# Kernel tuning notes

Measured on AMD Instinct MI355X. Metric: run time of the kernel, lower is better.

Reference implementation:

```python
import jax, jax.numpy as jnp
import numpy as np

N_ROIS = 8192
C, S = 256, 7
D = C * S * S  # 12544 flattened RoI feature dim
NUM_CLASSES = 31
DIMS = {"cls": NUM_CLASSES + 1, "reg": 4 * NUM_CLASSES, "face": 3, "colour": 7, "motion": 2}


def setup_inputs() -> dict:
    key = jax.random.key(0)
    ks = jax.random.split(key, 6)
    x = jax.random.normal(ks[0], (N_ROIS, C, S, S), dtype=jnp.float32)
    inp = {"x": x}
    for i, (name, out_dim) in enumerate(DIMS.items()):
        inp[f"W_{name}"] = 0.01 * jax.random.normal(ks[i + 1], (D, out_dim), dtype=jnp.float32)
        inp[f"b_{name}"] = jnp.zeros((out_dim,), dtype=jnp.float32)
    return inp


def reference(x, W_cls, b_cls, W_reg, b_reg, W_face, b_face,
              W_colour, b_colour, W_motion, b_motion):
    # AttributeBBoxHead.forward with with_avg_pool=False: flatten then 5 linear heads.
    xf = x.reshape(x.shape[0], -1)  # (N, 12544)
    cls_score = xf @ W_cls + b_cls        # (N, 32)
    bbox_pred = xf @ W_reg + b_reg        # (N, 124)
    face_score = xf @ W_face + b_face     # (N, 3)
    colour_score = xf @ W_colour + b_colour  # (N, 7)
    motion_score = xf @ W_motion + b_motion  # (N, 2)
    return (cls_score, bbox_pred, face_score, colour_score, motion_score)
```

## Files before the change

### kernel.cpp

```cpp
#include <hip/hip_runtime.h>
#include <hip/hip_bf16.h>
#include <stdint.h>

#define D_DIM 12544
#define NROIS 8192
#define NCOLS 168
#define NCPAD 176
#define NT 11
#define SPLIT 8
#define KSPLIT (D_DIM / SPLIT)
#define BK 32
#define KITERS (KSPLIT / BK)
#define BM 64

#define XROW_B 72
#define WCOL_B 80
#define WL_COLS 192
#define XL_BYTES (BM * XROW_B)
#define WL_BYTES (WL_COLS * WCOL_B)
#define BUF_BYTES (XL_BYTES + WL_BYTES)

typedef __attribute__((ext_vector_type(8))) short short8;
typedef __attribute__((ext_vector_type(4))) float floatx4;

__device__ __forceinline__ uint32_t pk_bf16(float a, float b) {
    uint32_t ua = __float_as_uint(a);
    uint32_t ub = __float_as_uint(b);
    ua = (ua + 0x7FFFu + ((ua >> 16) & 1u)) >> 16;
    ub = (ub + 0x7FFFu + ((ub >> 16) & 1u)) >> 16;
    return ua | (ub << 16);
}

__global__ __launch_bounds__(256) void pack_w(
        const float* __restrict__ Wc, const float* __restrict__ Wr,
        const float* __restrict__ Wf, const float* __restrict__ Wco,
        const float* __restrict__ Wm, uint16_t* __restrict__ Wp) {
    __shared__ float tile[64][33];
    int k0 = blockIdx.x * 64;
    int c0 = blockIdx.y * 32;
    int t  = threadIdx.x;

    int rc = t & 31;
    int rk = t >> 5;
#pragma unroll
    for (int rr = 0; rr < 8; ++rr) {
        int k = rr * 8 + rk;
        int kk = k0 + k;
        int c = c0 + rc;
        float v = 0.f;
        if (c < 32)       v = Wc[(size_t)kk * 32  + c];
        else if (c < 156) v = Wr[(size_t)kk * 124 + (c - 32)];
        else if (c < 159) v = Wf[(size_t)kk * 3   + (c - 156)];
        else if (c < 166) v = Wco[(size_t)kk * 7  + (c - 159)];
        else if (c < 168) v = Wm[(size_t)kk * 2   + (c - 166)];
        tile[k][rc] = v;
    }
    __syncthreads();

    int wc = t >> 3;
    int wk = t & 7;
    int c  = c0 + wc;
    if (c < NCPAD) {
        uint32_t o[4];
#pragma unroll
        for (int j = 0; j < 4; ++j)
            o[j] = pk_bf16(tile[wk * 8 + 2 * j][wc], tile[wk * 8 + 2 * j + 1][wc]);
        uint4 v = make_uint4(o[0], o[1], o[2], o[3]);
        *(uint4*)(Wp + (size_t)c * D_DIM + k0 + wk * 8) = v;
    }
}

__global__ __launch_bounds__(256) void gemm_split(const float* __restrict__ X,
                                                  const uint16_t* __restrict__ Wp,
                                                  uint16_t* __restrict__ parts) {
    __shared__ __attribute__((aligned(16))) char lds[2 * BUF_BYTES];

    int b     = blockIdx.x;
    int split = b & 7;
    int rb    = b >> 3;
    int row0  = rb * BM;
    int kbase = split * KSPLIT;

    int t    = threadIdx.x;
    int wave = t >> 6;
    int lane = t & 63;

    int sx_row = t >> 2;
    int sx_kc  = t & 3;
    const float* xg = X + (size_t)(row0 + sx_row) * D_DIM + kbase + sx_kc * 8;

    int sw_col = t >> 2;
    int sw_ch  = t & 3;
    int c0g = sw_col       < NCPAD ? sw_col       : NCPAD - 1;
    int c1g = sw_col + 64  < NCPAD ? sw_col + 64  : NCPAD - 1;
    int c2g = sw_col + 128 < NCPAD ? sw_col + 128 : NCPAD - 1;
    const uint16_t* wg0 = Wp + (size_t)c0g * D_DIM + kbase + sw_ch * 8;
    const uint16_t* wg1 = Wp + (size_t)c1g * D_DIM + kbase + sw_ch * 8;
    const uint16_t* wg2 = Wp + (size_t)c2g * D_DIM + kbase + sw_ch * 8;

    int x_st = sx_row * XROW_B + sx_kc * 16;
    int w_st0 = XL_BYTES + (sw_col)       * WCOL_B + sw_ch * 16;
    int w_st1 = XL_BYTES + (sw_col + 64)  * WCOL_B + sw_ch * 16;
    int w_st2 = XL_BYTES + (sw_col + 128) * WCOL_B + sw_ch * 16;

    int n    = lane & 15;
    int quad = lane >> 4;
    int xf_off = (wave * 16 + n) * XROW_B + quad * 16;
    int wf_off = XL_BYTES + n * WCOL_B + quad * 16;

    floatx4 acc[NT];
#pragma unroll
    for (int tt = 0; tt < NT; ++tt) acc[tt] = (floatx4)0.f;

    float4 px0 = *(const float4*)xg;
    float4 px1 = *(const float4*)(xg + 4);
    xg += BK;
    short8 pw0 = *(const short8*)wg0; wg0 += BK;
    short8 pw1 = *(const short8*)wg1; wg1 += BK;
    short8 pw2 = *(const short8*)wg2; wg2 += BK;
    {
        union { uint32_t u[4]; short8 s; } p;
        p.u[0] = pk_bf16(px0.x, px0.y); p.u[1] = pk_bf16(px0.z, px0.w);
        p.u[2] = pk_bf16(px1.x, px1.y); p.u[3] = pk_bf16(px1.z, px1.w);
        *(short8*)(lds + x_st) = p.s;
        *(short8*)(lds + w_st0) = pw0;
        *(short8*)(lds + w_st1) = pw1;
        *(short8*)(lds + w_st2) = pw2;
    }
    int cur = 0;

    for (int it = 0; it < KITERS; ++it) {
        __syncthreads();

        float4 nx0, nx1; short8 nw0, nw1, nw2;
        bool more = (it + 1 < KITERS);
        if (more) {
            nx0 = *(const float4*)xg;
            nx1 = *(const float4*)(xg + 4);
            xg += BK;
            nw0 = *(const short8*)wg0; wg0 += BK;
            nw1 = *(const short8*)wg1; wg1 += BK;
            nw2 = *(const short8*)wg2; wg2 += BK;
        }

        const char* cb = lds + cur * BUF_BYTES;
        short8 xf = *(const short8*)(cb + xf_off);
#pragma unroll
        for (int tt = 0; tt < NT; ++tt) {
            short8 wf = *(const short8*)(cb + wf_off + tt * (16 * WCOL_B));
            acc[tt] = __builtin_amdgcn_mfma_f32_16x16x32_bf16(wf, xf, acc[tt], 0, 0, 0);
        }

        if (more) {
            char* nb = lds + (cur ^ 1) * BUF_BYTES;
            union { uint32_t u[4]; short8 s; } p;
            p.u[0] = pk_bf16(nx0.x, nx0.y); p.u[1] = pk_bf16(nx0.z, nx0.w);
            p.u[2] = pk_bf16(nx1.x, nx1.y); p.u[3] = pk_bf16(nx1.z, nx1.w);
            *(short8*)(nb + x_st) = p.s;
            *(short8*)(nb + w_st0) = nw0;
            *(short8*)(nb + w_st1) = nw1;
            *(short8*)(nb + w_st2) = nw2;
            cur ^= 1;
        }
    }

    uint16_t* pb = parts + ((size_t)split * NROIS + row0 + wave * 16 + n) * NCOLS;
#pragma unroll
    for (int tt = 0; tt < NT; ++tt) {
        int col0 = tt * 16 + quad * 4;
        if (col0 + 3 < NCOLS) {
            uint32_t lo = pk_bf16(acc[tt].x, acc[tt].y);
            uint32_t hi = pk_bf16(acc[tt].z, acc[tt].w);
            uint2 v = make_uint2(lo, hi);
            *(uint2*)(pb + col0) = v;
        }
    }
}

__global__ void reduce_out(const uint16_t* __restrict__ parts,
                           const float* __restrict__ bc, const float* __restrict__ br,
                           const float* __restrict__ bf, const float* __restrict__ bco,
                           const float* __restrict__ bm, float* __restrict__ out) {
    int r = blockIdx.x;
    int c = threadIdx.x;
    if (c >= NCOLS) return;
    const size_t S = (size_t)NROIS * NCOLS;
    size_t off = (size_t)r * NCOLS + c;
    float v = 0.f;
#pragma unroll
    for (int s = 0; s < SPLIT; ++s)
        v += __uint_as_float((uint32_t)parts[off + (size_t)s * S] << 16);
    float bias; size_t oidx;
    if (c < 32)       { bias = bc[c];        oidx = (size_t)r * 32  + c; }
    else if (c < 156) { bias = br[c - 32];   oidx = 262144u  + (size_t)r * 124 + (c - 32); }
    else if (c < 159) { bias = bf[c - 156];  oidx = 1277952u + (size_t)r * 3   + (c - 156); }
    else if (c < 166) { bias = bco[c - 159]; oidx = 1302528u + (size_t)r * 7   + (c - 159); }
    else              { bias = bm[c - 166];  oidx = 1359872u + (size_t)r * 2   + (c - 166); }
    out[oidx] = v + bias;
}

extern "C" void kernel_launch(void* const* d_in, const int* in_sizes, int n_in,
                              void* d_out, int out_size, void* d_ws, size_t ws_size,
                              hipStream_t stream) {
    const float* X   = (const float*)d_in[0];
    const float* Wc  = (const float*)d_in[1];
    const float* bc  = (const float*)d_in[2];
    const float* Wr  = (const float*)d_in[3];
    const float* br  = (const float*)d_in[4];
    const float* Wf  = (const float*)d_in[5];
    const float* bfa = (const float*)d_in[6];
    const float* Wco = (const float*)d_in[7];
    const float* bco = (const float*)d_in[8];
    const float* Wm  = (const float*)d_in[9];
    const float* bm  = (const float*)d_in[10];

    uint16_t* Wp    = (uint16_t*)d_ws;
    uint16_t* parts = (uint16_t*)((char*)d_ws + (size_t)NCPAD * D_DIM * 2);
    float* out = (float*)d_out;

    pack_w<<<dim3(D_DIM / 64, 6), 256, 0, stream>>>(Wc, Wr, Wf, Wco, Wm, Wp);
    gemm_split<<<1024, 256, 0, stream>>>(X, Wp, parts);
    reduce_out<<<NROIS, 192, 0, stream>>>(parts, bc, br, bfa, bco, bm, out);
}
```

Before: 608.8 us.

## Load X fragments directly to registers and fuse split-K reduction via tickets

X tiles are no longer staged through shared memory. Each lane loads its own MFMA fragment from global memory and converts it to bf16 in registers, which cuts LDS traffic and footprint. The separate reduce kernel is removed: each row block counts finished K-splits with an atomic ticket, and the last block sums the partials and adds bias. This saves a launch and a pass over partials, but adds fence and atomic overhead and leaves the final reduction to a single block per row group.

```diff
diff --git a/kernel.cpp b/kernel.cpp
--- a/kernel.cpp
+++ b/kernel.cpp
@@ -1,5 +1,4 @@
 #include <hip/hip_runtime.h>
-#include <hip/hip_bf16.h>
 #include <stdint.h>
 
 #define D_DIM 12544
@@ -12,13 +11,11 @@
 #define BK 32
 #define KITERS (KSPLIT / BK)
 #define BM 64
-
-#define XROW_B 72
+#define NRB (NROIS / BM)
+
 #define WCOL_B 80
 #define WL_COLS 192
-#define XL_BYTES (BM * XROW_B)
-#define WL_BYTES (WL_COLS * WCOL_B)
-#define BUF_BYTES (XL_BYTES + WL_BYTES)
+#define WBUF_BYTES (WL_COLS * WCOL_B)
 
 typedef __attribute__((ext_vector_type(8))) short short8;
 typedef __attribute__((ext_vector_type(4))) float floatx4;
@@ -34,11 +31,14 @@
 __global__ __launch_bounds__(256) void pack_w(
         const float* __restrict__ Wc, const float* __restrict__ Wr,
         const float* __restrict__ Wf, const float* __restrict__ Wco,
-        const float* __restrict__ Wm, uint16_t* __restrict__ Wp) {
+        const float* __restrict__ Wm, uint16_t* __restrict__ Wp,
+        uint32_t* __restrict__ tickets) {
     __shared__ float tile[64][33];
     int k0 = blockIdx.x * 64;
     int c0 = blockIdx.y * 32;
     int t  = threadIdx.x;
+
+    if (blockIdx.x == 0 && blockIdx.y == 0 && t < NRB) tickets[t] = 0;
 
     int rc = t & 31;
     int rk = t >> 5;
@@ -70,10 +70,14 @@
     }
 }
 
-__global__ __launch_bounds__(256) void gemm_split(const float* __restrict__ X,
-                                                  const uint16_t* __restrict__ Wp,
-                                                  uint16_t* __restrict__ parts) {
-    __shared__ __attribute__((aligned(16))) char lds[2 * BUF_BYTES];
+__global__ __launch_bounds__(256) void gemm_fused(
+        const float* __restrict__ X, const uint16_t* __restrict__ Wp,
+        uint16_t* __restrict__ parts, uint32_t* __restrict__ tickets,
+        const float* __restrict__ bc, const float* __restrict__ br,
+        const float* __restrict__ bfa, const float* __restrict__ bco,
+        const float* __restrict__ bm, float* __restrict__ out) {
+    __shared__ __attribute__((aligned(16))) char lds[2 * WBUF_BYTES];
+    __shared__ uint32_t s_ticket;
 
     int b     = blockIdx.x;
     int split = b & 7;
@@ -84,10 +88,8 @@
     int t    = threadIdx.x;
     int wave = t >> 6;
     int lane = t & 63;
-
-    int sx_row = t >> 2;
-    int sx_kc  = t & 3;
-    const float* xg = X + (size_t)(row0 + sx_row) * D_DIM + kbase + sx_kc * 8;
+    int n    = lane & 15;
+    int quad = lane >> 4;
 
     int sw_col = t >> 2;
     int sw_ch  = t & 3;
@@ -97,16 +99,13 @@
     const uint16_t* wg0 = Wp + (size_t)c0g * D_DIM + kbase + sw_ch * 8;
     const uint16_t* wg1 = Wp + (size_t)c1g * D_DIM + kbase + sw_ch * 8;
     const uint16_t* wg2 = Wp + (size_t)c2g * D_DIM + kbase + sw_ch * 8;
-
-    int x_st = sx_row * XROW_B + sx_kc * 16;
-    int w_st0 = XL_BYTES + (sw_col)       * WCOL_B + sw_ch * 16;
-    int w_st1 = XL_BYTES + (sw_col + 64)  * WCOL_B + sw_ch * 16;
-    int w_st2 = XL_BYTES + (sw_col + 128) * WCOL_B + sw_ch * 16;
-
-    int n    = lane & 15;
-    int quad = lane >> 4;
-    int xf_off = (wave * 16 + n) * XROW_B + quad * 16;
-    int wf_off = XL_BYTES + n * WCOL_B + quad * 16;
+    int w_st0 = (sw_col)       * WCOL_B + sw_ch * 16;
+    int w_st1 = (sw_col + 64)  * WCOL_B + sw_ch * 16;
+    int w_st2 = (sw_col + 128) * WCOL_B + sw_ch * 16;
+
+    const float* xg = X + (size_t)(row0 + wave * 16 + n) * D_DIM + kbase + quad * 8;
+
+    int wf_off = n * WCOL_B + quad * 16;
 
     floatx4 acc[NT];
 #pragma unroll
@@ -115,14 +114,10 @@
     float4 px0 = *(const float4*)xg;
     float4 px1 = *(const float4*)(xg + 4);
     xg += BK;
-    short8 pw0 = *(const short8*)wg0; wg0 += BK;
-    short8 pw1 = *(const short8*)wg1; wg1 += BK;
-    short8 pw2 = *(const short8*)wg2; wg2 += BK;
     {
-        union { uint32_t u[4]; short8 s; } p;
-        p.u[0] = pk_bf16(px0.x, px0.y); p.u[1] = pk_bf16(px0.z, px0.w);
-        p.u[2] = pk_bf16(px1.x, px1.y); p.u[3] = pk_bf16(px1.z, px1.w);
-        *(short8*)(lds + x_st) = p.s;
+        short8 pw0 = *(const short8*)wg0; wg0 += BK;
+        short8 pw1 = *(const short8*)wg1; wg1 += BK;
+        short8 pw2 = *(const short8*)wg2; wg2 += BK;
         *(short8*)(lds + w_st0) = pw0;
         *(short8*)(lds + w_st1) = pw1;
         *(short8*)(lds + w_st2) = pw2;
@@ -143,8 +138,12 @@
             nw2 = *(const short8*)wg2; wg2 += BK;
         }
 
-        const char* cb = lds + cur * BUF_BYTES;
-        short8 xf = *(const short8*)(cb + xf_off);
+        union { uint32_t u[4]; short8 s; } xp;
+        xp.u[0] = pk_bf16(px0.x, px0.y); xp.u[1] = pk_bf16(px0.z, px0.w);
+        xp.u[2] = pk_bf16(px1.x, px1.y); xp.u[3] = pk_bf16(px1.z, px1.w);
+        short8 xf = xp.s;
+
+        const char* cb = lds + cur * WBUF_BYTES;
 #pragma unroll
         for (int tt = 0; tt < NT; ++tt) {
             short8 wf = *(const short8*)(cb + wf_off + tt * (16 * WCOL_B));
@@ -152,14 +151,11 @@
         }
 
         if (more) {
-            char* nb = lds + (cur ^ 1) * BUF_BYTES;
-            union { uint32_t u[4]; short8 s; } p;
-            p.u[0] = pk_bf16(nx0.x, nx0.y); p.u[1] = pk_bf16(nx0.z, nx0.w);
-            p.u[2] = pk_bf16(nx1.x, nx1.y); p.u[3] = pk_bf16(nx1.z, nx1.w);
-            *(short8*)(nb + x_st) = p.s;
+            char* nb = lds + (cur ^ 1) * WBUF_BYTES;
             *(short8*)(nb + w_st0) = nw0;
             *(short8*)(nb + w_st1) = nw1;
             *(short8*)(nb + w_st2) = nw2;
+            px0 = nx0; px1 = nx1;
             cur ^= 1;
         }
     }
@@ -175,28 +171,31 @@
             *(uint2*)(pb + col0) = v;
         }
     }
-}
-
-__global__ void reduce_out(const uint16_t* __restrict__ parts,
-                           const float* __restrict__ bc, const float* __restrict__ br,
-                           const float* __restrict__ bf, const float* __restrict__ bco,
-                           const float* __restrict__ bm, float* __restrict__ out) {
-    int r = blockIdx.x;
-    int c = threadIdx.x;
-    if (c >= NCOLS) return;
-    const size_t S = (size_t)NROIS * NCOLS;
-    size_t off = (size_t)r * NCOLS + c;
-    float v = 0.f;
-#pragma unroll
-    for (int s = 0; s < SPLIT; ++s)
-        v += __uint_as_float((uint32_t)parts[off + (size_t)s * S] << 16);
-    float bias; size_t oidx;
-    if (c < 32)       { bias = bc[c];        oidx = (size_t)r * 32  + c; }
-    else if (c < 156) { bias = br[c - 32];   oidx = 262144u  + (size_t)r * 124 + (c - 32); }
-    else if (c < 159) { bias = bf[c - 156];  oidx = 1277952u + (size_t)r * 3   + (c - 156); }
-    else if (c < 166) { bias = bco[c - 159]; oidx = 1302528u + (size_t)r * 7   + (c - 159); }
-    else              { bias = bm[c - 166];  oidx = 1359872u + (size_t)r * 2   + (c - 166); }
-    out[oidx] = v + bias;
+
+    __threadfence();
+    if (t == 0) s_ticket = atomicAdd(&tickets[rb], 1u);
+    __syncthreads();
+    if (s_ticket != SPLIT - 1) return;
+    __threadfence();
+
+    const size_t PS = (size_t)NROIS * NCOLS;
+    for (int idx = t; idx < BM * NCOLS; idx += 256) {
+        int r = idx / NCOLS;
+        int c = idx - r * NCOLS;
+        size_t off = (size_t)(row0 + r) * NCOLS + c;
+        float v = 0.f;
+#pragma unroll
+        for (int s = 0; s < SPLIT; ++s)
+            v += __uint_as_float((uint32_t)parts[off + (size_t)s * PS] << 16);
+        float bias; size_t oidx;
+        size_t rr = (size_t)(row0 + r);
+        if (c < 32)       { bias = bc[c];        oidx = rr * 32  + c; }
+        else if (c < 156) { bias = br[c - 32];   oidx = 262144u  + rr * 124 + (c - 32); }
+        else if (c < 159) { bias = bfa[c - 156]; oidx = 1277952u + rr * 3   + (c - 156); }
+        else if (c < 166) { bias = bco[c - 159]; oidx = 1302528u + rr * 7   + (c - 159); }
+        else              { bias = bm[c - 166];  oidx = 1359872u + rr * 2   + (c - 166); }
+        out[oidx] = v + bias;
+    }
 }
 
 extern "C" void kernel_launch(void* const* d_in, const int* in_sizes, int n_in,
@@ -216,9 +215,11 @@
 
     uint16_t* Wp    = (uint16_t*)d_ws;
     uint16_t* parts = (uint16_t*)((char*)d_ws + (size_t)NCPAD * D_DIM * 2);
+    uint32_t* tickets = (uint32_t*)((char*)d_ws + (size_t)NCPAD * D_DIM * 2
+                                    + (size_t)SPLIT * NROIS * NCOLS * 2);
     float* out = (float*)d_out;
 
-    pack_w<<<dim3(D_DIM / 64, 6), 256, 0, stream>>>(Wc, Wr, Wf, Wco, Wm, Wp);
-    gemm_split<<<1024, 256, 0, stream>>>(X, Wp, parts);
-    reduce_out<<<NROIS, 192, 0, stream>>>(parts, bc, br, bfa, bco, bm, out);
-}
+    pack_w<<<dim3(D_DIM / 64, 6), 256, 0, stream>>>(Wc, Wr, Wf, Wco, Wm, Wp, tickets);
+    gemm_fused<<<SPLIT * NRB, 256, 0, stream>>>(X, Wp, parts, tickets,
+                                                bc, br, bfa, bco, bm, out);
+}
```

Result: slower. 907.5 us (+49.1%).
